# Optimization experiments

Measured on AMD Instinct MI355X. Metric: run time of the kernel, lower is better.

The kernel has to match this reference:

```python
import jax, jax.numpy as jnp
import numpy as np

N_NODES = 50000
N_EDGES = 800000
N_FEAT = 128
HIDDEN = 128
N_CLASSES = 10
N_LAYERS = 3
N_GRAPHS = 512


def setup_inputs() -> dict:
    key = jax.random.key(0)
    ks = jax.random.split(key, 16)
    s = 1.0 / np.sqrt(HIDDEN)
    inp = {
        "x": jax.random.normal(ks[0], (N_NODES, N_FEAT), jnp.float32),
        "edge_index": jax.random.randint(ks[1], (2, N_EDGES), 0, N_NODES, jnp.int64),
        "batch": jnp.sort(jax.random.randint(ks[2], (N_NODES,), 0, N_GRAPHS, jnp.int64)),
        "num_graphs": N_GRAPHS,
        "conv1_wl": jax.random.normal(ks[3], (N_FEAT, HIDDEN), jnp.float32) * s,
        "conv1_wr": jax.random.normal(ks[4], (N_FEAT, HIDDEN), jnp.float32) * s,
        "conv1_b": jnp.zeros((HIDDEN,), jnp.float32),
        "convs_wl": jax.random.normal(ks[5], (N_LAYERS - 1, HIDDEN, HIDDEN), jnp.float32) * s,
        "convs_wr": jax.random.normal(ks[6], (N_LAYERS - 1, HIDDEN, HIDDEN), jnp.float32) * s,
        "convs_b": jnp.zeros((N_LAYERS - 1, HIDDEN), jnp.float32),
        "gate_w": jax.random.normal(ks[7], (HIDDEN, 1), jnp.float32) * s,
        "gate_b": jnp.zeros((1,), jnp.float32),
        "lin1_w": jax.random.normal(ks[8], (HIDDEN, HIDDEN), jnp.float32) * s,
        "lin1_b": jnp.zeros((HIDDEN,), jnp.float32),
        "lin2_w": jax.random.normal(ks[9], (HIDDEN, N_CLASSES), jnp.float32) * s,
        "lin2_b": jnp.zeros((N_CLASSES,), jnp.float32),
    }
    return inp


def _sage_conv(x, src, dst, inv_deg, wl, wr, b):
    # mean aggregation of source-node features at destination nodes
    agg = jax.ops.segment_sum(x[src], dst, num_segments=N_NODES)  # [N, d]
    agg = agg * inv_deg
    return agg @ wl + x @ wr + b


def _global_attention(x, batch, num_graphs, gate_w, gate_b):
    gate = (x @ gate_w + gate_b)[:, 0]                      # [N]
    m = jax.ops.segment_max(gate, batch, num_segments=num_graphs)
    m = jnp.where(jnp.isfinite(m), m, 0.0)
    g = jnp.exp(gate - m[batch])                            # stable segment softmax
    den = jax.ops.segment_sum(g, batch, num_segments=num_graphs)
    attn = g / den[batch]
    return jax.ops.segment_sum(attn[:, None] * x, batch, num_segments=num_graphs)


def reference(x, edge_index, batch, num_graphs,
              conv1_wl, conv1_wr, conv1_b,
              convs_wl, convs_wr, convs_b,
              gate_w, gate_b, lin1_w, lin1_b, lin2_w, lin2_b):
    src, dst = edge_index[0], edge_index[1]
    deg = jax.ops.segment_sum(jnp.ones((src.shape[0],), x.dtype), dst,
                              num_segments=N_NODES)
    inv_deg = (1.0 / jnp.maximum(deg, 1.0))[:, None]

    h = jax.nn.relu(_sage_conv(x, src, dst, inv_deg, conv1_wl, conv1_wr, conv1_b))
    for i in range(convs_wl.shape[0]):
        h = jax.nn.relu(_sage_conv(h, src, dst, inv_deg,
                                   convs_wl[i], convs_wr[i], convs_b[i]))

    pooled = _global_attention(h, batch, num_graphs, gate_w, gate_b)  # [G, H]
    out = jax.nn.relu(pooled @ lin1_w + lin1_b)
    # dropout p=0.5 is identity at eval time
    logits = out @ lin2_w + lin2_b
    return jax.nn.log_softmax(logits, axis=-1)
```

## Files before the change

### kernel.cpp

```cpp
#include <hip/hip_runtime.h>
#include <math.h>

#define N_NODES 50000
#define N_PAD   50048
#define N_EDGES 800000
#define FEAT 128
#define K2 256
#define N_GRAPHS 512
#define N_CLASSES 10
#define BCAP 64
#define BROW 264
#define OROW 72
#define AGG_BLOCKS 2048

#define FILL_BLOCKS 1000
#define FILL_ITER 25
#define RANGE_NODES 6250
#define CNT_STRIDE 16
#define PREP_BLOCKS (FILL_BLOCKS + 6250 + 384 + 3)

typedef __attribute__((ext_vector_type(8))) short short8;
typedef __attribute__((ext_vector_type(4))) float floatx4;

__device__ __forceinline__ float bflo(unsigned u) { return __uint_as_float(u << 16); }
__device__ __forceinline__ float bfhi(unsigned u) { return __uint_as_float(u & 0xffff0000u); }
__device__ __forceinline__ unsigned short f2bf(float f) {
    unsigned u = __float_as_uint(f);
    u = (u + 0x7fffu + ((u >> 16) & 1u)) >> 16;
    return (unsigned short)u;
}
__device__ __forceinline__ unsigned pack2(float a, float b) {
    return (unsigned)f2bf(a) | ((unsigned)f2bf(b) << 16);
}

__global__ __launch_bounds__(256) void prep_kernel(
    const int* __restrict__ src, const int* __restrict__ dst,
    int* __restrict__ cnt, unsigned short* __restrict__ bucket,
    const float* __restrict__ x, unsigned short* __restrict__ A,
    const float* __restrict__ wl1, const float* __restrict__ wr1,
    const float* __restrict__ wl23, const float* __restrict__ wr23,
    unsigned short* __restrict__ wt,
    const int* __restrict__ batch, int* __restrict__ goffs) {
    int b = blockIdx.x, t = threadIdx.x;
    if (b < FILL_BLOCKS) {
        int chunk = b >> 3, r = b & 7;
        int lo = r * RANGE_NODES, hi = lo + RANGE_NODES;
        int base = chunk * (FILL_ITER * 256) + t;
        for (int i = 0; i < FILL_ITER; ++i) {
            int e = base + i * 256;
            int d = dst[e];
            if (d >= lo && d < hi) {
                int p = atomicAdd(&cnt[d << 4], 1);
                if (p < BCAP) bucket[(size_t)d * BCAP + p] = (unsigned short)src[e];
            }
        }
    } else if (b < FILL_BLOCKS + 6250) {
        int idx = (b - FILL_BLOCKS) * 256 + t;
        if (idx < N_NODES * 32) {
            int n = idx >> 5, f4 = idx & 31;
            float4 v = ((const float4*)(x + (size_t)n * FEAT))[f4];
            uint2 o = make_uint2(pack2(v.x, v.y), pack2(v.z, v.w));
            *(uint2*)(A + (size_t)n * K2 + FEAT + f4 * 4) = o;
        }
    } else if (b < FILL_BLOCKS + 6250 + 384) {
        int idx = (b - FILL_BLOCKS - 6250) * 256 + t;
        int layer = idx >> 15;
        int r = idx & 32767;
        int n = r >> 8, k = r & 255;
        const float* wl = (layer == 0) ? wl1 : wl23 + (size_t)(layer - 1) * FEAT * FEAT;
        const float* wr = (layer == 0) ? wr1 : wr23 + (size_t)(layer - 1) * FEAT * FEAT;
        float v = (k < FEAT) ? wl[k * FEAT + n] : wr[(k - FEAT) * FEAT + n];
        wt[idx] = f2bf(v);
    } else {
        int g = (b - FILL_BLOCKS - 6250 - 384) * 256 + t;
        if (g > N_GRAPHS) return;
        int lo = 0, hi = N_NODES;
        while (lo < hi) {
            int mid = (lo + hi) >> 1;
            if (batch[mid] < g) lo = mid + 1; else hi = mid;
        }
        goffs[g] = lo;
    }
}

__device__ __forceinline__ void acc8(float* acc, uint4 u) {
    acc[0] += bflo(u.x); acc[1] += bfhi(u.x);
    acc[2] += bflo(u.y); acc[3] += bfhi(u.y);
    acc[4] += bflo(u.z); acc[5] += bfhi(u.z);
    acc[6] += bflo(u.w); acc[7] += bfhi(u.w);
}

__global__ __launch_bounds__(256) void aggregate_bf16(
    const unsigned short* __restrict__ hin, const int* __restrict__ cnt,
    const unsigned short* __restrict__ bucket, unsigned short* __restrict__ aggout) {
    int lane = threadIdx.x & 63;
    int g = lane >> 4;
    int l16 = lane & 15;
    int wid = (blockIdx.x << 2) + (threadIdx.x >> 6);
    const int nw = gridDim.x << 2;

    int n = wid;
    if (n >= N_NODES) return;
    int deg = cnt[n << 4];

    while (true) {
        const unsigned short* cp = bucket + (size_t)n * BCAP;
        int c = min(deg, BCAP);
        int nq = c >> 2;
        int rem = c & 3;

        int nn = n + nw;
        int dnext = 0;
        if (nn < N_NODES) {
            dnext = cnt[nn << 4];
            unsigned short bpre = bucket[(size_t)nn * BCAP + lane];
            asm volatile("" :: "v"((int)bpre));
        }

        float acc[8];
        #pragma unroll
        for (int i = 0; i < 8; ++i) acc[i] = 0.f;

        int i = 0;
        for (; i + 4 <= nq; i += 4) {
            int s0 = cp[i * 4 + g];
            int s1 = cp[i * 4 + 4 + g];
            int s2 = cp[i * 4 + 8 + g];
            int s3 = cp[i * 4 + 12 + g];
            uint4 u0 = *(const uint4*)(hin + (size_t)s0 * K2 + l16 * 8);
            uint4 u1 = *(const uint4*)(hin + (size_t)s1 * K2 + l16 * 8);
            uint4 u2 = *(const uint4*)(hin + (size_t)s2 * K2 + l16 * 8);
            uint4 u3 = *(const uint4*)(hin + (size_t)s3 * K2 + l16 * 8);
            acc8(acc, u0); acc8(acc, u1); acc8(acc, u2); acc8(acc, u3);
        }
        if (i + 2 <= nq) {
            int s0 = cp[i * 4 + g];
            int s1 = cp[i * 4 + 4 + g];
            uint4 u0 = *(const uint4*)(hin + (size_t)s0 * K2 + l16 * 8);
            uint4 u1 = *(const uint4*)(hin + (size_t)s1 * K2 + l16 * 8);
            acc8(acc, u0); acc8(acc, u1);
            i += 2;
        }
        if (i < nq) {
            int s0 = cp[i * 4 + g];
            uint4 u0 = *(const uint4*)(hin + (size_t)s0 * K2 + l16 * 8);
            acc8(acc, u0);
        }
        if (g < rem) {
            int s0 = cp[nq * 4 + g];
            uint4 u0 = *(const uint4*)(hin + (size_t)s0 * K2 + l16 * 8);
            acc8(acc, u0);
        }
        #pragma unroll
        for (int j = 0; j < 8; ++j) {
            acc[j] += __shfl_xor(acc[j], 16);
            acc[j] += __shfl_xor(acc[j], 32);
        }
        if (g == 0) {
            float inv = 1.0f / fmaxf((float)deg, 1.0f);
            uint4 o;
            o.x = pack2(acc[0] * inv, acc[1] * inv);
            o.y = pack2(acc[2] * inv, acc[3] * inv);
            o.z = pack2(acc[4] * inv, acc[5] * inv);
            o.w = pack2(acc[6] * inv, acc[7] * inv);
            *(uint4*)(aggout + (size_t)n * K2 + l16 * 8) = o;
        }
        if (nn >= N_NODES) break;
        n = nn;
        deg = dnext;
    }
}

__global__ __launch_bounds__(256) void gemm_mfma(
    const unsigned short* __restrict__ Ain, unsigned short* __restrict__ Aout,
    const unsigned short* __restrict__ Wt, const float* __restrict__ bias,
    const float* __restrict__ gate_w, float* __restrict__ gate) {
    __shared__ unsigned short sB[64 * BROW];
    __shared__ unsigned short sOut[4][32 * OROW];
    int t = threadIdx.x;
    int wave = t >> 6, lane = t & 63;
    int q = lane >> 4, l16 = lane & 15;

    const int nwg_q = 97, nwg_r = 6;
    int orig = blockIdx.x;
    int xcd = orig & 7, idx = orig >> 3;
    int wgid = (xcd < nwg_r) ? xcd * (nwg_q + 1) + idx
                             : nwg_r * (nwg_q + 1) + (xcd - nwg_r) * nwg_q + idx;
    int tileM = wgid >> 1;
    int nh = wgid & 1;
    int row0 = tileM * 128 + wave * 32;

    const unsigned short* pa0 = Ain + (size_t)(row0 + l16) * K2 + q * 8;
    const unsigned short* pa1 = pa0 + 16 * K2;
    short8 a0[8], a1[8];
    #pragma unroll
    for (int ks = 0; ks < 8; ++ks) {
        a0[ks] = *(const short8*)(pa0 + ks * 32);
        a1[ks] = *(const short8*)(pa1 + ks * 32);
    }

    #pragma unroll
    for (int i = 0; i < 8; ++i) {
        int flat = i * 256 + t;
        int rw = flat >> 5, fr = flat & 31;
        uint4 v = *((const uint4*)(Wt + (size_t)(nh * 64 + rw) * K2) + fr);
        *(uint4*)(&sB[rw * BROW + fr * 8]) = v;
    }
    __syncthreads();

    floatx4 acc[2][4];
    #pragma unroll
    for (int i = 0; i < 2; ++i)
        #pragma unroll
        for (int j = 0; j < 4; ++j) acc[i][j] = (floatx4){0.f, 0.f, 0.f, 0.f};

    #pragma unroll
    for (int ks = 0; ks < 8; ++ks) {
        #pragma unroll
        for (int nb = 0; nb < 4; ++nb) {
            short8 b = *(const short8*)(&sB[(nb * 16 + l16) * BROW + ks * 32 + q * 8]);
            acc[0][nb] = __builtin_amdgcn_mfma_f32_16x16x32_bf16(a0[ks], b, acc[0][nb], 0, 0, 0);
            acc[1][nb] = __builtin_amdgcn_mfma_f32_16x16x32_bf16(a1[ks], b, acc[1][nb], 0, 0, 0);
        }
    }

    float bv[4], gwv[4];
    #pragma unroll
    for (int nb = 0; nb < 4; ++nb) bv[nb] = bias[nh * 64 + nb * 16 + l16];
    if (gate_w) {
        #pragma unroll
        for (int nb = 0; nb < 4; ++nb) gwv[nb] = gate_w[nh * 64 + nb * 16 + l16];
    }

    #pragma unroll
    for (int band = 0; band < 2; ++band) {
        #pragma unroll
        for (int r = 0; r < 4; ++r) {
            int lr = band * 16 + q * 4 + r;
            float gsum = 0.f;
            #pragma unroll
            for (int nb = 0; nb < 4; ++nb) {
                float v = fmaxf(acc[band][nb][r] + bv[nb], 0.f);
                sOut[wave][lr * OROW + nb * 16 + l16] = f2bf(v);
                if (gate_w) gsum += v * gwv[nb];
            }
            if (gate_w) {
                gsum += __shfl_xor(gsum, 1);
                gsum += __shfl_xor(gsum, 2);
                gsum += __shfl_xor(gsum, 4);
                gsum += __shfl_xor(gsum, 8);
                int m = row0 + lr;
                if (l16 == 0 && m < N_NODES) atomicAdd(&gate[m], gsum);
            }
        }
    }

    int r2 = lane >> 1, h2 = lane & 1;
    size_t gbase = (size_t)(row0 + r2) * K2 + FEAT + nh * 64 + h2 * 32;
    #pragma unroll
    for (int j = 0; j < 2; ++j) {
        uint4 v0 = *(uint4*)(&sOut[wave][r2 * OROW + h2 * 32 + j * 16]);
        uint4 v1 = *(uint4*)(&sOut[wave][r2 * OROW + h2 * 32 + j * 16 + 8]);
        *(uint4*)(Aout + gbase + j * 16) = v0;
        *(uint4*)(Aout + gbase + j * 16 + 8) = v1;
    }
}

__global__ __launch_bounds__(256) void pool_head(
    const unsigned short* __restrict__ h, const float* __restrict__ gate,
    const int* __restrict__ goffs,
    const float* __restrict__ w1, const float* __restrict__ b1,
    const float* __restrict__ w2, const float* __restrict__ b2,
    float* __restrict__ out) {
    __shared__ float sred[4];
    __shared__ float facc[4][128];
    __shared__ float pv[128], qv[128], lg[N_CLASSES];
    int g = blockIdx.x;
    int s = goffs[g], e = goffs[g + 1];
    int t = threadIdx.x;
    int wave = t >> 6, lane = t & 63;

    if (s < e) {
        float mx = -INFINITY;
        for (int n = s + t; n < e; n += 256) mx = fmaxf(mx, gate[n]);
        #pragma unroll
        for (int off = 32; off; off >>= 1) mx = fmaxf(mx, __shfl_xor(mx, off));
        if (lane == 0) sred[wave] = mx;
        __syncthreads();
        float m = fmaxf(fmaxf(sred[0], sred[1]), fmaxf(sred[2], sred[3]));
        __syncthreads();
        float d = 0.f;
        for (int n = s + t; n < e; n += 256) d += __expf(gate[n] - m);
        #pragma unroll
        for (int off = 32; off; off >>= 1) d += __shfl_xor(d, off);
        if (lane == 0) sred[wave] = d;
        __syncthreads();
        float den = sred[0] + sred[1] + sred[2] + sred[3];
        float acc0 = 0.f, acc1 = 0.f;
        for (int n = s + wave; n < e; n += 4) {
            float gn = __expf(gate[n] - m);
            unsigned u = *(const unsigned*)(h + (size_t)n * K2 + lane * 2);
            acc0 += gn * bflo(u);
            acc1 += gn * bfhi(u);
        }
        facc[wave][lane * 2]     = acc0;
        facc[wave][lane * 2 + 1] = acc1;
        __syncthreads();
        if (t < 128) pv[t] = (facc[0][t] + facc[1][t] + facc[2][t] + facc[3][t]) / den;
    } else {
        if (t < 128) pv[t] = 0.f;
    }
    __syncthreads();

    if (t < 128) {
        float acc = b1[t];
        #pragma unroll 4
        for (int k = 0; k < 128; ++k) acc += pv[k] * w1[k * FEAT + t];
        qv[t] = fmaxf(acc, 0.f);
    }
    __syncthreads();
    if (t < N_CLASSES) {
        float a = b2[t];
        #pragma unroll 4
        for (int k = 0; k < 128; ++k) a += qv[k] * w2[k * N_CLASSES + t];
        lg[t] = a;
    }
    __syncthreads();
    if (t < N_CLASSES) {
        float m = -INFINITY;
        #pragma unroll
        for (int j = 0; j < N_CLASSES; ++j) m = fmaxf(m, lg[j]);
        float sum = 0.f;
        #pragma unroll
        for (int j = 0; j < N_CLASSES; ++j) sum += __expf(lg[j] - m);
        out[(size_t)g * N_CLASSES + t] = lg[t] - m - __logf(sum);
    }
}

static inline size_t align256(size_t x) { return (x + 255) & ~(size_t)255; }

extern "C" void kernel_launch(void* const* d_in, const int* in_sizes, int n_in,
                              void* d_out, int out_size, void* d_ws, size_t ws_size,
                              hipStream_t stream) {
    const float* x        = (const float*)d_in[0];
    const int*   ei       = (const int*)d_in[1];
    const int*   batch    = (const int*)d_in[2];
    const float* conv1_wl = (const float*)d_in[4];
    const float* conv1_wr = (const float*)d_in[5];
    const float* conv1_b  = (const float*)d_in[6];
    const float* convs_wl = (const float*)d_in[7];
    const float* convs_wr = (const float*)d_in[8];
    const float* convs_b  = (const float*)d_in[9];
    const float* gate_w   = (const float*)d_in[10];
    const float* lin1_w   = (const float*)d_in[12];
    const float* lin1_b   = (const float*)d_in[13];
    const float* lin2_w   = (const float*)d_in[14];
    const float* lin2_b   = (const float*)d_in[15];
    float* out = (float*)d_out;

    const int* src = ei;
    const int* dst = ei + N_EDGES;

    char* w = (char*)d_ws;
    size_t off = 0;
    unsigned short* A0   = (unsigned short*)(w + off); off += align256((size_t)N_PAD * K2 * 2);
    unsigned short* A1   = (unsigned short*)(w + off); off += align256((size_t)N_PAD * K2 * 2);
    unsigned short* bkt  = (unsigned short*)(w + off); off += align256((size_t)N_NODES * BCAP * 2);
    unsigned short* wt   = (unsigned short*)(w + off); off += align256((size_t)3 * FEAT * K2 * 2);
    int*   i_goff = (int*)(w + off);   off += align256((size_t)(N_GRAPHS + 1) * 4);
    char* zbase = w + off;
    int*   i_cnt  = (int*)(w + off);   off += align256((size_t)N_NODES * CNT_STRIDE * 4);
    float* f_gate = (float*)(w + off); off += align256((size_t)N_NODES * 4);
    size_t zbytes = (size_t)((w + off) - zbase);

    hipMemsetAsync(zbase, 0, zbytes, stream);

    prep_kernel<<<PREP_BLOCKS, 256, 0, stream>>>(
        src, dst, i_cnt, bkt,
        x, A0, conv1_wl, conv1_wr, convs_wl, convs_wr, wt, batch, i_goff);

    const int GB = (N_PAD / 128) * 2;

    aggregate_bf16<<<AGG_BLOCKS, 256, 0, stream>>>(A0 + FEAT, i_cnt, bkt, A0);
    gemm_mfma<<<GB, 256, 0, stream>>>(A0, A1, wt, conv1_b, nullptr, nullptr);
    aggregate_bf16<<<AGG_BLOCKS, 256, 0, stream>>>(A1 + FEAT, i_cnt, bkt, A1);
    gemm_mfma<<<GB, 256, 0, stream>>>(A1, A0, wt + FEAT * K2, convs_b, nullptr, nullptr);
    aggregate_bf16<<<AGG_BLOCKS, 256, 0, stream>>>(A0 + FEAT, i_cnt, bkt, A0);
    gemm_mfma<<<GB, 256, 0, stream>>>(A0, A1, wt + 2 * FEAT * K2, convs_b + FEAT,
                                      gate_w, f_gate);

    pool_head<<<N_GRAPHS, 256, 0, stream>>>(A1 + FEAT, f_gate, i_goff,
                                            lin1_w, lin1_b, lin2_w, lin2_b, out);
}
```

Measured before the change: 291.7 us.

## Software-pipeline neighbor gathers across nodes and simplify CSR bucket fill

The aggregation kernel now issues a fixed batch of eight neighbor-row loads for the next node before it reduces the current node. Slots past a node's degree reuse its last valid neighbor and are given zero weight, and double-buffered registers hide gather latency. The bucket fill in the prep kernel drops the destination-range partitioning with its repeated passes and uses one edge per thread with atomics. This raises register pressure, and low-degree nodes still pay for redundant loads. Atomic contention and the order of bucket entries also change.

```diff
diff --git a/kernel.cpp b/kernel.cpp
--- a/kernel.cpp
+++ b/kernel.cpp
@@ -12,12 +12,11 @@
 #define BROW 264
 #define OROW 72
 #define AGG_BLOCKS 2048
-
-#define FILL_BLOCKS 1000
-#define FILL_ITER 25
-#define RANGE_NODES 6250
+#define QFIX 8
 #define CNT_STRIDE 16
-#define PREP_BLOCKS (FILL_BLOCKS + 6250 + 384 + 3)
+
+#define FILLB 3125
+#define PREP_BLOCKS (FILLB + 6250 + 384 + 3)
 
 typedef __attribute__((ext_vector_type(8))) short short8;
 typedef __attribute__((ext_vector_type(4))) float floatx4;
@@ -42,28 +41,21 @@
     unsigned short* __restrict__ wt,
     const int* __restrict__ batch, int* __restrict__ goffs) {
     int b = blockIdx.x, t = threadIdx.x;
-    if (b < FILL_BLOCKS) {
-        int chunk = b >> 3, r = b & 7;
-        int lo = r * RANGE_NODES, hi = lo + RANGE_NODES;
-        int base = chunk * (FILL_ITER * 256) + t;
-        for (int i = 0; i < FILL_ITER; ++i) {
-            int e = base + i * 256;
-            int d = dst[e];
-            if (d >= lo && d < hi) {
-                int p = atomicAdd(&cnt[d << 4], 1);
-                if (p < BCAP) bucket[(size_t)d * BCAP + p] = (unsigned short)src[e];
-            }
-        }
-    } else if (b < FILL_BLOCKS + 6250) {
-        int idx = (b - FILL_BLOCKS) * 256 + t;
+    if (b < FILLB) {
+        int e = b * 256 + t;
+        int d = dst[e];
+        int p = atomicAdd(&cnt[d << 4], 1);
+        if (p < BCAP) bucket[(size_t)d * BCAP + p] = (unsigned short)src[e];
+    } else if (b < FILLB + 6250) {
+        int idx = (b - FILLB) * 256 + t;
         if (idx < N_NODES * 32) {
             int n = idx >> 5, f4 = idx & 31;
             float4 v = ((const float4*)(x + (size_t)n * FEAT))[f4];
             uint2 o = make_uint2(pack2(v.x, v.y), pack2(v.z, v.w));
             *(uint2*)(A + (size_t)n * K2 + FEAT + f4 * 4) = o;
         }
-    } else if (b < FILL_BLOCKS + 6250 + 384) {
-        int idx = (b - FILL_BLOCKS - 6250) * 256 + t;
+    } else if (b < FILLB + 6250 + 384) {
+        int idx = (b - FILLB - 6250) * 256 + t;
         int layer = idx >> 15;
         int r = idx & 32767;
         int n = r >> 8, k = r & 255;
@@ -72,7 +64,7 @@
         float v = (k < FEAT) ? wl[k * FEAT + n] : wr[(k - FEAT) * FEAT + n];
         wt[idx] = f2bf(v);
     } else {
-        int g = (b - FILL_BLOCKS - 6250 - 384) * 256 + t;
+        int g = (b - FILLB - 6250 - 384) * 256 + t;
         if (g > N_GRAPHS) return;
         int lo = 0, hi = N_NODES;
         while (lo < hi) {
@@ -89,6 +81,72 @@
     acc[4] += bflo(u.z); acc[5] += bfhi(u.z);
     acc[6] += bflo(u.w); acc[7] += bfhi(u.w);
 }
+__device__ __forceinline__ void acc8w(float* acc, uint4 u, float w) {
+    acc[0] = fmaf(bflo(u.x), w, acc[0]); acc[1] = fmaf(bfhi(u.x), w, acc[1]);
+    acc[2] = fmaf(bflo(u.y), w, acc[2]); acc[3] = fmaf(bfhi(u.y), w, acc[3]);
+    acc[4] = fmaf(bflo(u.z), w, acc[4]); acc[5] = fmaf(bfhi(u.z), w, acc[5]);
+    acc[6] = fmaf(bflo(u.w), w, acc[6]); acc[7] = fmaf(bfhi(u.w), w, acc[7]);
+}
+
+#define AGG_WARM(node, degv)                                                  \
+    if ((node) < N_NODES) {                                                   \
+        degv = cnt[(node) << 4];                                              \
+        unsigned short t_ = bucket[(size_t)(node) * BCAP + lane];             \
+        asm volatile("" :: "v"((int)t_));                                     \
+    }
+
+#define AGG_ISSUE(U, node, degv)                                              \
+    {                                                                         \
+        const unsigned short* cp_ = bucket + (size_t)(node) * BCAP;           \
+        int c_ = min(degv, BCAP);                                             \
+        int cm_ = max(c_ - 1, 0);                                             \
+        _Pragma("unroll")                                                     \
+        for (int i_ = 0; i_ < QFIX; ++i_) {                                   \
+            int sl_ = cp_[min(i_ * 4 + g, cm_)];                              \
+            U[i_] = *(const uint4*)(hin + (size_t)sl_ * K2 + l16 * 8);        \
+        }                                                                     \
+    }
+
+#define AGG_CONSUME(U, node, degv)                                            \
+    {                                                                         \
+        const unsigned short* cp_ = bucket + (size_t)(node) * BCAP;           \
+        int c_ = min(degv, BCAP);                                             \
+        float acc_[8];                                                        \
+        _Pragma("unroll") for (int j_ = 0; j_ < 8; ++j_) acc_[j_] = 0.f;      \
+        if (c_ > 4 * QFIX) {                              \
+            int nq_ = c_ >> 2;                                                \
+            for (int i_ = QFIX; i_ < nq_; ++i_) {                             \
+                int sl_ = cp_[i_ * 4 + g];                                    \
+                uint4 u_ = *(const uint4*)(hin + (size_t)sl_ * K2 + l16 * 8); \
+                acc8(acc_, u_);                                               \
+            }                                                                 \
+            int rem_ = c_ & 3;                                                \
+            if (g < rem_) {                                                   \
+                int sl_ = cp_[nq_ * 4 + g];                                   \
+                uint4 u_ = *(const uint4*)(hin + (size_t)sl_ * K2 + l16 * 8); \
+                acc8(acc_, u_);                                               \
+            }                                                                 \
+        }                                                                     \
+        _Pragma("unroll")                                                     \
+        for (int i_ = 0; i_ < QFIX; ++i_) {                                   \
+            float w_ = (i_ * 4 + g < c_) ? 1.f : 0.f;                         \
+            acc8w(acc_, U[i_], w_);                                           \
+        }                                                                     \
+        _Pragma("unroll")                                                     \
+        for (int j_ = 0; j_ < 8; ++j_) {                                      \
+            acc_[j_] += __shfl_xor(acc_[j_], 16);                             \
+            acc_[j_] += __shfl_xor(acc_[j_], 32);                             \
+        }                                                                     \
+        if (g == 0) {                                                         \
+            float inv_ = 1.0f / fmaxf((float)(degv), 1.0f);                   \
+            uint4 o_;                                                         \
+            o_.x = pack2(acc_[0] * inv_, acc_[1] * inv_);                     \
+            o_.y = pack2(acc_[2] * inv_, acc_[3] * inv_);                     \
+            o_.z = pack2(acc_[4] * inv_, acc_[5] * inv_);                     \
+            o_.w = pack2(acc_[6] * inv_, acc_[7] * inv_);                     \
+            *(uint4*)(aggout + (size_t)(node) * K2 + l16 * 8) = o_;           \
+        }                                                                     \
+    }
 
 __global__ __launch_bounds__(256) void aggregate_bf16(
     const unsigned short* __restrict__ hin, const int* __restrict__ cnt,
@@ -98,76 +156,31 @@
     int l16 = lane & 15;
     int wid = (blockIdx.x << 2) + (threadIdx.x >> 6);
     const int nw = gridDim.x << 2;
-
-    int n = wid;
-    if (n >= N_NODES) return;
-    int deg = cnt[n << 4];
-
-    while (true) {
-        const unsigned short* cp = bucket + (size_t)n * BCAP;
-        int c = min(deg, BCAP);
-        int nq = c >> 2;
-        int rem = c & 3;
-
-        int nn = n + nw;
-        int dnext = 0;
-        if (nn < N_NODES) {
-            dnext = cnt[nn << 4];
-            unsigned short bpre = bucket[(size_t)nn * BCAP + lane];
-            asm volatile("" :: "v"((int)bpre));
-        }
-
-        float acc[8];
-        #pragma unroll
-        for (int i = 0; i < 8; ++i) acc[i] = 0.f;
-
-        int i = 0;
-        for (; i + 4 <= nq; i += 4) {
-            int s0 = cp[i * 4 + g];
-            int s1 = cp[i * 4 + 4 + g];
-            int s2 = cp[i * 4 + 8 + g];
-            int s3 = cp[i * 4 + 12 + g];
-            uint4 u0 = *(const uint4*)(hin + (size_t)s0 * K2 + l16 * 8);
-            uint4 u1 = *(const uint4*)(hin + (size_t)s1 * K2 + l16 * 8);
-            uint4 u2 = *(const uint4*)(hin + (size_t)s2 * K2 + l16 * 8);
-            uint4 u3 = *(const uint4*)(hin + (size_t)s3 * K2 + l16 * 8);
-            acc8(acc, u0); acc8(acc, u1); acc8(acc, u2); acc8(acc, u3);
-        }
-        if (i + 2 <= nq) {
-            int s0 = cp[i * 4 + g];
-            int s1 = cp[i * 4 + 4 + g];
-            uint4 u0 = *(const uint4*)(hin + (size_t)s0 * K2 + l16 * 8);
-            uint4 u1 = *(const uint4*)(hin + (size_t)s1 * K2 + l16 * 8);
-            acc8(acc, u0); acc8(acc, u1);
-            i += 2;
-        }
-        if (i < nq) {
-            int s0 = cp[i * 4 + g];
-            uint4 u0 = *(const uint4*)(hin + (size_t)s0 * K2 + l16 * 8);
-            acc8(acc, u0);
-        }
-        if (g < rem) {
-            int s0 = cp[nq * 4 + g];
-            uint4 u0 = *(const uint4*)(hin + (size_t)s0 * K2 + l16 * 8);
-            acc8(acc, u0);
-        }
-        #pragma unroll
-        for (int j = 0; j < 8; ++j) {
-            acc[j] += __shfl_xor(acc[j], 16);
-            acc[j] += __shfl_xor(acc[j], 32);
-        }
-        if (g == 0) {
-            float inv = 1.0f / fmaxf((float)deg, 1.0f);
-            uint4 o;
-            o.x = pack2(acc[0] * inv, acc[1] * inv);
-            o.y = pack2(acc[2] * inv, acc[3] * inv);
-            o.z = pack2(acc[4] * inv, acc[5] * inv);
-            o.w = pack2(acc[6] * inv, acc[7] * inv);
-            *(uint4*)(aggout + (size_t)n * K2 + l16 * 8) = o;
-        }
-        if (nn >= N_NODES) break;
-        n = nn;
-        deg = dnext;
+    if (wid >= N_NODES) return;
+
+    uint4 uA[QFIX], uB[QFIX];
+
+    int n0 = wid;
+    int d0 = cnt[n0 << 4];
+    int n1 = n0 + nw;
+    int d1 = 0;
+    AGG_WARM(n1, d1);
+    AGG_ISSUE(uA, n0, d0);
+
+    for (;;) {
+        if (n1 >= N_NODES) { AGG_CONSUME(uA, n0, d0); break; }
+        int n2 = n1 + nw;
+        int d2 = 0;
+        AGG_WARM(n2, d2);
+        AGG_ISSUE(uB, n1, d1);
+        AGG_CONSUME(uA, n0, d0);
+        if (n2 >= N_NODES) { AGG_CONSUME(uB, n1, d1); break; }
+        int n3 = n2 + nw;
+        int d3 = 0;
+        AGG_WARM(n3, d3);
+        AGG_ISSUE(uA, n2, d2);
+        AGG_CONSUME(uB, n1, d1);
+        n0 = n2; d0 = d2; n1 = n3; d1 = d3;
     }
 }
 
```

New measurement: 412.7 us. 41.5% more time.

## Compute both GEMM column halves per block and write gate directly; simplify edge fill

Applied to the files above, without the earlier changes.

Each GEMM workgroup now processes both 64-column halves of the output in sequence, halving the grid to 391 blocks. Because the full gate dot product is accumulated in registers, it can be stored directly instead of atomically added, so the gate buffer no longer needs zeroing by the memset. The bucket fill also switches from range-partitioned blocks, each scanning 25 edge iterations, to one edge per thread over 3125 blocks, which removes the redundant dst reads. The trade-offs are fewer parallel GEMM blocks, a second weight load into LDS behind an extra barrier in each block, and more random atomic traffic across the whole node range.

```diff
diff --git a/kernel.cpp b/kernel.cpp
--- a/kernel.cpp
+++ b/kernel.cpp
@@ -12,12 +12,10 @@
 #define BROW 264
 #define OROW 72
 #define AGG_BLOCKS 2048
-
-#define FILL_BLOCKS 1000
-#define FILL_ITER 25
-#define RANGE_NODES 6250
 #define CNT_STRIDE 16
-#define PREP_BLOCKS (FILL_BLOCKS + 6250 + 384 + 3)
+
+#define FILLB 3125
+#define PREP_BLOCKS (FILLB + 6250 + 384 + 3)
 
 typedef __attribute__((ext_vector_type(8))) short short8;
 typedef __attribute__((ext_vector_type(4))) float floatx4;
@@ -42,28 +40,21 @@
     unsigned short* __restrict__ wt,
     const int* __restrict__ batch, int* __restrict__ goffs) {
     int b = blockIdx.x, t = threadIdx.x;
-    if (b < FILL_BLOCKS) {
-        int chunk = b >> 3, r = b & 7;
-        int lo = r * RANGE_NODES, hi = lo + RANGE_NODES;
-        int base = chunk * (FILL_ITER * 256) + t;
-        for (int i = 0; i < FILL_ITER; ++i) {
-            int e = base + i * 256;
-            int d = dst[e];
-            if (d >= lo && d < hi) {
-                int p = atomicAdd(&cnt[d << 4], 1);
-                if (p < BCAP) bucket[(size_t)d * BCAP + p] = (unsigned short)src[e];
-            }
-        }
-    } else if (b < FILL_BLOCKS + 6250) {
-        int idx = (b - FILL_BLOCKS) * 256 + t;
+    if (b < FILLB) {
+        int e = b * 256 + t;
+        int d = dst[e];
+        int p = atomicAdd(&cnt[d << 4], 1);
+        if (p < BCAP) bucket[(size_t)d * BCAP + p] = (unsigned short)src[e];
+    } else if (b < FILLB + 6250) {
+        int idx = (b - FILLB) * 256 + t;
         if (idx < N_NODES * 32) {
             int n = idx >> 5, f4 = idx & 31;
             float4 v = ((const float4*)(x + (size_t)n * FEAT))[f4];
             uint2 o = make_uint2(pack2(v.x, v.y), pack2(v.z, v.w));
             *(uint2*)(A + (size_t)n * K2 + FEAT + f4 * 4) = o;
         }
-    } else if (b < FILL_BLOCKS + 6250 + 384) {
-        int idx = (b - FILL_BLOCKS - 6250) * 256 + t;
+    } else if (b < FILLB + 6250 + 384) {
+        int idx = (b - FILLB - 6250) * 256 + t;
         int layer = idx >> 15;
         int r = idx & 32767;
         int n = r >> 8, k = r & 255;
@@ -72,7 +63,7 @@
         float v = (k < FEAT) ? wl[k * FEAT + n] : wr[(k - FEAT) * FEAT + n];
         wt[idx] = f2bf(v);
     } else {
-        int g = (b - FILL_BLOCKS - 6250 - 384) * 256 + t;
+        int g = (b - FILLB - 6250 - 384) * 256 + t;
         if (g > N_GRAPHS) return;
         int lo = 0, hi = N_NODES;
         while (lo < hi) {
@@ -181,14 +172,12 @@
     int wave = t >> 6, lane = t & 63;
     int q = lane >> 4, l16 = lane & 15;
 
-    const int nwg_q = 97, nwg_r = 6;
+    const int nwg_q = 48, nwg_r = 7;
     int orig = blockIdx.x;
     int xcd = orig & 7, idx = orig >> 3;
     int wgid = (xcd < nwg_r) ? xcd * (nwg_q + 1) + idx
                              : nwg_r * (nwg_q + 1) + (xcd - nwg_r) * nwg_q + idx;
-    int tileM = wgid >> 1;
-    int nh = wgid & 1;
-    int row0 = tileM * 128 + wave * 32;
+    int row0 = wgid * 128 + wave * 32;
 
     const unsigned short* pa0 = Ain + (size_t)(row0 + l16) * K2 + q * 8;
     const unsigned short* pa1 = pa0 + 16 * K2;
@@ -199,70 +188,88 @@
         a1[ks] = *(const short8*)(pa1 + ks * 32);
     }
 
+    float gsum[2][4];
     #pragma unroll
-    for (int i = 0; i < 8; ++i) {
-        int flat = i * 256 + t;
-        int rw = flat >> 5, fr = flat & 31;
-        uint4 v = *((const uint4*)(Wt + (size_t)(nh * 64 + rw) * K2) + fr);
-        *(uint4*)(&sB[rw * BROW + fr * 8]) = v;
-    }
-    __syncthreads();
-
-    floatx4 acc[2][4];
-    #pragma unroll
-    for (int i = 0; i < 2; ++i)
-        #pragma unroll
-        for (int j = 0; j < 4; ++j) acc[i][j] = (floatx4){0.f, 0.f, 0.f, 0.f};
-
-    #pragma unroll
-    for (int ks = 0; ks < 8; ++ks) {
-        #pragma unroll
-        for (int nb = 0; nb < 4; ++nb) {
-            short8 b = *(const short8*)(&sB[(nb * 16 + l16) * BROW + ks * 32 + q * 8]);
-            acc[0][nb] = __builtin_amdgcn_mfma_f32_16x16x32_bf16(a0[ks], b, acc[0][nb], 0, 0, 0);
-            acc[1][nb] = __builtin_amdgcn_mfma_f32_16x16x32_bf16(a1[ks], b, acc[1][nb], 0, 0, 0);
-        }
-    }
-
-    float bv[4], gwv[4];
-    #pragma unroll
-    for (int nb = 0; nb < 4; ++nb) bv[nb] = bias[nh * 64 + nb * 16 + l16];
-    if (gate_w) {
-        #pragma unroll
-        for (int nb = 0; nb < 4; ++nb) gwv[nb] = gate_w[nh * 64 + nb * 16 + l16];
-    }
-
-    #pragma unroll
-    for (int band = 0; band < 2; ++band) {
-        #pragma unroll
-        for (int r = 0; r < 4; ++r) {
-            int lr = band * 16 + q * 4 + r;
-            float gsum = 0.f;
+    for (int b_ = 0; b_ < 2; ++b_)
+        #pragma unroll
+        for (int r_ = 0; r_ < 4; ++r_) gsum[b_][r_] = 0.f;
+
+    for (int nh = 0; nh < 2; ++nh) {
+        if (nh) __syncthreads();
+        #pragma unroll
+        for (int i = 0; i < 8; ++i) {
+            int flat = i * 256 + t;
+            int rw = flat >> 5, fr = flat & 31;
+            uint4 v = *((const uint4*)(Wt + (size_t)(nh * 64 + rw) * K2) + fr);
+            *(uint4*)(&sB[rw * BROW + fr * 8]) = v;
+        }
+        __syncthreads();
+
+        floatx4 acc[2][4];
+        #pragma unroll
+        for (int i = 0; i < 2; ++i)
+            #pragma unroll
+            for (int j = 0; j < 4; ++j) acc[i][j] = (floatx4){0.f, 0.f, 0.f, 0.f};
+
+        #pragma unroll
+        for (int ks = 0; ks < 8; ++ks) {
             #pragma unroll
             for (int nb = 0; nb < 4; ++nb) {
-                float v = fmaxf(acc[band][nb][r] + bv[nb], 0.f);
-                sOut[wave][lr * OROW + nb * 16 + l16] = f2bf(v);
-                if (gate_w) gsum += v * gwv[nb];
+                short8 b = *(const short8*)(&sB[(nb * 16 + l16) * BROW + ks * 32 + q * 8]);
+                acc[0][nb] = __builtin_amdgcn_mfma_f32_16x16x32_bf16(a0[ks], b, acc[0][nb], 0, 0, 0);
+                acc[1][nb] = __builtin_amdgcn_mfma_f32_16x16x32_bf16(a1[ks], b, acc[1][nb], 0, 0, 0);
             }
-            if (gate_w) {
-                gsum += __shfl_xor(gsum, 1);
-                gsum += __shfl_xor(gsum, 2);
-                gsum += __shfl_xor(gsum, 4);
-                gsum += __shfl_xor(gsum, 8);
-                int m = row0 + lr;
-                if (l16 == 0 && m < N_NODES) atomicAdd(&gate[m], gsum);
+        }
+
+        float bv[4], gwv[4];
+        #pragma unroll
+        for (int nb = 0; nb < 4; ++nb) bv[nb] = bias[nh * 64 + nb * 16 + l16];
+        if (gate_w) {
+            #pragma unroll
+            for (int nb = 0; nb < 4; ++nb) gwv[nb] = gate_w[nh * 64 + nb * 16 + l16];
+        }
+
+        #pragma unroll
+        for (int band = 0; band < 2; ++band) {
+            #pragma unroll
+            for (int r = 0; r < 4; ++r) {
+                int lr = band * 16 + q * 4 + r;
+                float gs = 0.f;
+                #pragma unroll
+                for (int nb = 0; nb < 4; ++nb) {
+                    float v = fmaxf(acc[band][nb][r] + bv[nb], 0.f);
+                    sOut[wave][lr * OROW + nb * 16 + l16] = f2bf(v);
+                    if (gate_w) gs += v * gwv[nb];
+                }
+                if (gate_w) gsum[band][r] += gs;
             }
         }
-    }
-
-    int r2 = lane >> 1, h2 = lane & 1;
-    size_t gbase = (size_t)(row0 + r2) * K2 + FEAT + nh * 64 + h2 * 32;
-    #pragma unroll
-    for (int j = 0; j < 2; ++j) {
-        uint4 v0 = *(uint4*)(&sOut[wave][r2 * OROW + h2 * 32 + j * 16]);
-        uint4 v1 = *(uint4*)(&sOut[wave][r2 * OROW + h2 * 32 + j * 16 + 8]);
-        *(uint4*)(Aout + gbase + j * 16) = v0;
-        *(uint4*)(Aout + gbase + j * 16 + 8) = v1;
+
+        int r2 = lane >> 1, h2 = lane & 1;
+        size_t gbase = (size_t)(row0 + r2) * K2 + FEAT + nh * 64 + h2 * 32;
+        #pragma unroll
+        for (int j = 0; j < 2; ++j) {
+            uint4 v0 = *(uint4*)(&sOut[wave][r2 * OROW + h2 * 32 + j * 16]);
+            uint4 v1 = *(uint4*)(&sOut[wave][r2 * OROW + h2 * 32 + j * 16 + 8]);
+            *(uint4*)(Aout + gbase + j * 16) = v0;
+            *(uint4*)(Aout + gbase + j * 16 + 8) = v1;
+        }
+    }
+
+    if (gate_w) {
+        #pragma unroll
+        for (int band = 0; band < 2; ++band) {
+            #pragma unroll
+            for (int r = 0; r < 4; ++r) {
+                float gs = gsum[band][r];
+                gs += __shfl_xor(gs, 1);
+                gs += __shfl_xor(gs, 2);
+                gs += __shfl_xor(gs, 4);
+                gs += __shfl_xor(gs, 8);
+                int m = row0 + band * 16 + q * 4 + r;
+                if (l16 == 0 && m < N_NODES) gate[m] = gs;
+            }
+        }
     }
 }
 
@@ -370,8 +377,8 @@
     int*   i_goff = (int*)(w + off);   off += align256((size_t)(N_GRAPHS + 1) * 4);
     char* zbase = w + off;
     int*   i_cnt  = (int*)(w + off);   off += align256((size_t)N_NODES * CNT_STRIDE * 4);
+    size_t zbytes = (size_t)((w + off) - zbase);
     float* f_gate = (float*)(w + off); off += align256((size_t)N_NODES * 4);
-    size_t zbytes = (size_t)((w + off) - zbase);
 
     hipMemsetAsync(zbase, 0, zbytes, stream);
 
@@ -379,7 +386,7 @@
         src, dst, i_cnt, bkt,
         x, A0, conv1_wl, conv1_wr, convs_wl, convs_wr, wt, batch, i_goff);
 
-    const int GB = (N_PAD / 128) * 2;
+    const int GB = N_PAD / 128;
 
     aggregate_bf16<<<AGG_BLOCKS, 256, 0, stream>>>(A0 + FEAT, i_cnt, bkt, A0);
     gemm_mfma<<<GB, 256, 0, stream>>>(A0, A1, wt, conv1_b, nullptr, nullptr);
```

After: 297.1 us. No clear change (+1.8%).

## Simplify edge bucket fill and alias GEMM output staging onto B tile LDS

Applied to the files above, without the earlier changes.

The bucket fill in the prep kernel no longer makes each chunk scan its edges eight times, once per destination-node range. It now launches one thread per edge that does its atomic slot claim directly, which cuts redundant dst reads but gives up the locality of range-partitioned atomics. In the GEMM kernel, the per-wave output staging buffer now reuses the shared memory of the B tile after a barrier, shrinking LDS per block. Launch bounds now request four blocks per CU to raise occupancy, at the cost of an extra __syncthreads and possible register pressure.

```diff
diff --git a/kernel.cpp b/kernel.cpp
--- a/kernel.cpp
+++ b/kernel.cpp
@@ -12,12 +12,10 @@
 #define BROW 264
 #define OROW 72
 #define AGG_BLOCKS 2048
-
-#define FILL_BLOCKS 1000
-#define FILL_ITER 25
-#define RANGE_NODES 6250
 #define CNT_STRIDE 16
-#define PREP_BLOCKS (FILL_BLOCKS + 6250 + 384 + 3)
+
+#define FILLB 3125
+#define PREP_BLOCKS (FILLB + 6250 + 384 + 3)
 
 typedef __attribute__((ext_vector_type(8))) short short8;
 typedef __attribute__((ext_vector_type(4))) float floatx4;
@@ -42,28 +40,21 @@
     unsigned short* __restrict__ wt,
     const int* __restrict__ batch, int* __restrict__ goffs) {
     int b = blockIdx.x, t = threadIdx.x;
-    if (b < FILL_BLOCKS) {
-        int chunk = b >> 3, r = b & 7;
-        int lo = r * RANGE_NODES, hi = lo + RANGE_NODES;
-        int base = chunk * (FILL_ITER * 256) + t;
-        for (int i = 0; i < FILL_ITER; ++i) {
-            int e = base + i * 256;
-            int d = dst[e];
-            if (d >= lo && d < hi) {
-                int p = atomicAdd(&cnt[d << 4], 1);
-                if (p < BCAP) bucket[(size_t)d * BCAP + p] = (unsigned short)src[e];
-            }
-        }
-    } else if (b < FILL_BLOCKS + 6250) {
-        int idx = (b - FILL_BLOCKS) * 256 + t;
+    if (b < FILLB) {
+        int e = b * 256 + t;
+        int d = dst[e];
+        int p = atomicAdd(&cnt[d << 4], 1);
+        if (p < BCAP) bucket[(size_t)d * BCAP + p] = (unsigned short)src[e];
+    } else if (b < FILLB + 6250) {
+        int idx = (b - FILLB) * 256 + t;
         if (idx < N_NODES * 32) {
             int n = idx >> 5, f4 = idx & 31;
             float4 v = ((const float4*)(x + (size_t)n * FEAT))[f4];
             uint2 o = make_uint2(pack2(v.x, v.y), pack2(v.z, v.w));
             *(uint2*)(A + (size_t)n * K2 + FEAT + f4 * 4) = o;
         }
-    } else if (b < FILL_BLOCKS + 6250 + 384) {
-        int idx = (b - FILL_BLOCKS - 6250) * 256 + t;
+    } else if (b < FILLB + 6250 + 384) {
+        int idx = (b - FILLB - 6250) * 256 + t;
         int layer = idx >> 15;
         int r = idx & 32767;
         int n = r >> 8, k = r & 255;
@@ -72,7 +63,7 @@
         float v = (k < FEAT) ? wl[k * FEAT + n] : wr[(k - FEAT) * FEAT + n];
         wt[idx] = f2bf(v);
     } else {
-        int g = (b - FILL_BLOCKS - 6250 - 384) * 256 + t;
+        int g = (b - FILLB - 6250 - 384) * 256 + t;
         if (g > N_GRAPHS) return;
         int lo = 0, hi = N_NODES;
         while (lo < hi) {
@@ -171,15 +162,17 @@
     }
 }
 
-__global__ __launch_bounds__(256) void gemm_mfma(
+__global__ __launch_bounds__(256, 4) void gemm_mfma(
     const unsigned short* __restrict__ Ain, unsigned short* __restrict__ Aout,
     const unsigned short* __restrict__ Wt, const float* __restrict__ bias,
     const float* __restrict__ gate_w, float* __restrict__ gate) {
-    __shared__ unsigned short sB[64 * BROW];
-    __shared__ unsigned short sOut[4][32 * OROW];
+    __shared__ __align__(16) char smem[64 * BROW * 2];
+    unsigned short* sB = (unsigned short*)smem;
+    unsigned short* sOutW;
     int t = threadIdx.x;
     int wave = t >> 6, lane = t & 63;
     int q = lane >> 4, l16 = lane & 15;
+    sOutW = (unsigned short*)smem + wave * 32 * OROW;
 
     const int nwg_q = 97, nwg_r = 6;
     int orig = blockIdx.x;
@@ -223,6 +216,7 @@
             acc[1][nb] = __builtin_amdgcn_mfma_f32_16x16x32_bf16(a1[ks], b, acc[1][nb], 0, 0, 0);
         }
     }
+    __syncthreads();
 
     float bv[4], gwv[4];
     #pragma unroll
@@ -241,7 +235,7 @@
             #pragma unroll
             for (int nb = 0; nb < 4; ++nb) {
                 float v = fmaxf(acc[band][nb][r] + bv[nb], 0.f);
-                sOut[wave][lr * OROW + nb * 16 + l16] = f2bf(v);
+                sOutW[lr * OROW + nb * 16 + l16] = f2bf(v);
                 if (gate_w) gsum += v * gwv[nb];
             }
             if (gate_w) {
@@ -259,8 +253,8 @@
     size_t gbase = (size_t)(row0 + r2) * K2 + FEAT + nh * 64 + h2 * 32;
     #pragma unroll
     for (int j = 0; j < 2; ++j) {
-        uint4 v0 = *(uint4*)(&sOut[wave][r2 * OROW + h2 * 32 + j * 16]);
-        uint4 v1 = *(uint4*)(&sOut[wave][r2 * OROW + h2 * 32 + j * 16 + 8]);
+        uint4 v0 = *(uint4*)(&sOutW[r2 * OROW + h2 * 32 + j * 16]);
+        uint4 v1 = *(uint4*)(&sOutW[r2 * OROW + h2 * 32 + j * 16 + 8]);
         *(uint4*)(Aout + gbase + j * 16) = v0;
         *(uint4*)(Aout + gbase + j * 16 + 8) = v1;
     }
```

Result: slower. 302.7 us (+3.8%).
